# Optimization experiments

Hardware: AMD Instinct MI355X
Metric: run time of the kernel (lower is better)

Reference implementation:

```python
import jax, jax.numpy as jnp
import numpy as np

E = 64          # embedding_dim
H = 2 * E       # GRU hidden = input size = 128
ATT_HID = 36    # activation-unit MLP hidden


def _gru_scan(x, Wih, Whh, bih, bhh):
    """Standard (PyTorch-convention) GRU over x:[B,T,D] -> outputs [B,T,H]."""
    B = x.shape[0]
    gx = jnp.einsum('btd,gd->btg', x, Wih) + bih        # [B,T,3H], precompute input gates
    gx = jnp.swapaxes(gx, 0, 1)                          # [T,B,3H]
    h0 = jnp.zeros((B, H), x.dtype)

    def step(h, g):
        gh = h @ Whh.T + bhh                             # [B,3H]
        xr, xz, xn = jnp.split(g, 3, axis=-1)
        hr, hz, hn = jnp.split(gh, 3, axis=-1)
        r = jax.nn.sigmoid(xr + hr)
        z = jax.nn.sigmoid(xz + hz)
        n = jnp.tanh(xn + r * hn)
        h = (1.0 - z) * n + z * h
        return h, h

    _, hs = jax.lax.scan(step, h0, gx)                   # [T,B,H]
    return jnp.swapaxes(hs, 0, 1)                        # [B,T,H]


def _augru_scan(x, att, Wih, Whh, bih, bhh):
    """AUGRU: attention score scales the update gate. x:[B,T,H], att:[B,T]."""
    B = x.shape[0]
    gx = jnp.einsum('btd,gd->btg', x, Wih) + bih         # [B,T,3H]
    gx = jnp.swapaxes(gx, 0, 1)                          # [T,B,3H]
    a = jnp.swapaxes(att, 0, 1)[..., None]               # [T,B,1]
    h0 = jnp.zeros((B, H), x.dtype)

    def step(h, inp):
        g, at = inp
        gh = h @ Whh.T + bhh
        xr, xz, xn = jnp.split(g, 3, axis=-1)
        hr, hz, hn = jnp.split(gh, 3, axis=-1)
        r = jax.nn.sigmoid(xr + hr)
        u = jax.nn.sigmoid(xz + hz) * at                 # attention-modulated update gate
        n = jnp.tanh(xn + r * hn)
        h = (1.0 - u) * h + u * n
        return h, h

    _, hs = jax.lax.scan(step, h0, (gx, a))
    return jnp.swapaxes(hs, 0, 1)                        # [B,T,H]


def _attention_scores(query, hist, mask, W1, b1, W2, b2):
    """DIN activation unit: MLP over [q, h, q-h, q*h] -> masked softmax over T."""
    q = jnp.broadcast_to(query[:, None, :], hist.shape)  # [B,T,H]
    feat = jnp.concatenate([q, hist, q - hist, q * hist], axis=-1)  # [B,T,4H]
    hidden = jax.nn.sigmoid(jnp.einsum('btf,uf->btu', feat, W1) + b1)
    logits = (jnp.einsum('btu,ou->bto', hidden, W2) + b2)[..., 0]    # [B,T]
    logits = jnp.where(mask > 0, logits, -1e9)
    return jax.nn.softmax(logits, axis=-1)


def setup_inputs() -> dict:
    key = jax.random.key(0)
    ks = jax.random.split(key, 12)
    B, T = 1024, 200
    query_ad = jax.random.normal(ks[0], (B, H), jnp.float32)
    user_behavior = jax.random.normal(ks[1], (B, T, H), jnp.float32)
    lengths = jax.random.randint(ks[2], (B,), 1, T + 1)
    mask = (jnp.arange(T)[None, :] < lengths[:, None]).astype(jnp.int32)
    s = 1.0 / np.sqrt(H)
    p = {
        'gru_Wih': jax.random.uniform(ks[3], (3 * H, H), jnp.float32, -s, s),
        'gru_Whh': jax.random.uniform(ks[4], (3 * H, H), jnp.float32, -s, s),
        'gru_bih': jnp.zeros((3 * H,), jnp.float32),
        'gru_bhh': jnp.zeros((3 * H,), jnp.float32),
        'att_W1': jax.random.normal(ks[5], (ATT_HID, 4 * H), jnp.float32) * 0.05,
        'att_b1': jnp.zeros((ATT_HID,), jnp.float32),
        'att_W2': jax.random.normal(ks[6], (1, ATT_HID), jnp.float32) * 0.05,
        'att_b2': jnp.zeros((1,), jnp.float32),
        'augru_Wih': jax.random.uniform(ks[7], (3 * H, H), jnp.float32, -s, s),
        'augru_Whh': jax.random.uniform(ks[8], (3 * H, H), jnp.float32, -s, s),
        'augru_bih': jnp.zeros((3 * H,), jnp.float32),
        'augru_bhh': jnp.zeros((3 * H,), jnp.float32),
    }
    return dict(query_ad=query_ad, user_behavior=user_behavior, mask=mask, **p)


def reference(query_ad, user_behavior, mask,
              gru_Wih, gru_Whh, gru_bih, gru_bhh,
              att_W1, att_b1, att_W2, att_b2,
              augru_Wih, augru_Whh, augru_bih, augru_bhh):
    hist = _gru_scan(user_behavior, gru_Wih, gru_Whh, gru_bih, gru_bhh)       # [B,T,H]
    att = _attention_scores(query_ad, hist, mask, att_W1, att_b1, att_W2, att_b2)  # [B,T]
    out = _augru_scan(hist, att, augru_Wih, augru_Whh, augru_bih, augru_bhh)  # [B,T,H]
    lengths = jnp.sum(mask, axis=1)                                            # [B]
    B = out.shape[0]
    return out[jnp.arange(B), lengths - 1]                                     # [B,H]
```

## Files before the change

### kernel.cpp

```cpp
#include <hip/hip_runtime.h>

typedef _Float16 f16;
typedef _Float16 f16x8 __attribute__((ext_vector_type(8)));
typedef _Float16 f16x4 __attribute__((ext_vector_type(4)));
typedef float    f32x4 __attribute__((ext_vector_type(4)));

#define H  128
#define G3 384
#define AH 36
#define PADW 136

__device__ __forceinline__ float sigmoidf_(float x){
  return __builtin_amdgcn_rcpf(1.f + __expf(-x));
}
__device__ __forceinline__ float tanhf_(float x){
  return fmaf(2.f, __builtin_amdgcn_rcpf(1.f + __expf(-2.f*x)), -1.f);
}

__device__ __forceinline__ void lds_sync(){
  asm volatile("s_waitcnt lgkmcnt(0)" ::: "memory");
  __builtin_amdgcn_s_barrier();
  asm volatile("" ::: "memory");
}

__global__ void prep_weights(const float* __restrict__ a, const float* __restrict__ b,
                             const float* __restrict__ c, const float* __restrict__ d,
                             f16* __restrict__ dst)
{
  int i = blockIdx.x * 256 + threadIdx.x;
  if (i >= 4 * G3 * H) return;
  int m = i / (G3 * H), j = i % (G3 * H);
  const float* s = (m == 0) ? a : (m == 1) ? b : (m == 2) ? c : d;
  dst[i] = (f16)s[j];
}

__global__ void prep_len(const int* __restrict__ mask, int* __restrict__ len, int T, int B)
{
  int b = blockIdx.x * 256 + threadIdx.x;
  if (b >= B) return;
  int s = 0;
  for (int t = 0; t < T; ++t) s += (mask[(size_t)b * T + t] > 0);
  len[b] = s;
}

template<bool AUG>
__global__ __launch_bounds__(512)
__attribute__((amdgpu_waves_per_eu(2, 2)))
void scan_kernel(const float* __restrict__ xf32,
                 const f16*   __restrict__ xf16,
                 const f16*   __restrict__ Wih,
                 const f16*   __restrict__ Whh,
                 const float* __restrict__ bih,
                 const float* __restrict__ bhh,
                 const float* __restrict__ att,
                 const int*   __restrict__ len,
                 f16*         __restrict__ histo,
                 float*       __restrict__ outp,
                 int T)
{
  __shared__ f16  xs[2][16 * PADW];
  __shared__ f16  hs[2][16 * PADW];

  const int tid = threadIdx.x;
  const int w   = tid >> 6;
  const int l   = tid & 63;
  const int l16 = l & 15;
  const int lhi = l >> 4;
  const int b0  = blockIdx.x * 16;
  const int colb = w * 16;
  const int c4   = colb + lhi * 4;
  const int srow = tid >> 5, cc = tid & 31;

  f16x8 wih[3][4], whh[3][4];
  #pragma unroll
  for (int g = 0; g < 3; ++g)
    #pragma unroll
    for (int q = 0; q < 4; ++q) {
      int off = (g * H + colb + l16) * H + q * 32 + lhi * 8;
      wih[g][q] = *(const f16x8*)(Wih + off);
      whh[g][q] = *(const f16x8*)(Whh + off);
    }
  #pragma unroll
  for (int g = 0; g < 3; ++g)
    #pragma unroll
    for (int q = 0; q < 4; ++q)
      asm volatile("" : "+v"(wih[g][q]), "+v"(whh[g][q]));

  f32x4 bR  = *(const f32x4*)(bih + c4);
  { f32x4 t2 = *(const f32x4*)(bhh + c4);      bR  += t2; }
  f32x4 bZ  = *(const f32x4*)(bih + H + c4);
  { f32x4 t2 = *(const f32x4*)(bhh + H + c4);  bZ  += t2; }
  f32x4 bXn = *(const f32x4*)(bih + 2*H + c4);
  f32x4 bHn = *(const f32x4*)(bhh + 2*H + c4);

  float hold[4] = {0.f, 0.f, 0.f, 0.f};
  int len_l = 0;
  if (AUG) len_l = len[b0 + l16];

  const f16* xrd0 = &xs[0][l16 * PADW + lhi * 8];
  const f16* xrd1 = &xs[1][l16 * PADW + lhi * 8];
  const f16* hrd0 = &hs[0][l16 * PADW + lhi * 8];
  const f16* hrd1 = &hs[1][l16 * PADW + lhi * 8];
  f16* hwr0 = &hs[0][l16 * PADW + c4];
  f16* hwr1 = &hs[1][l16 * PADW + c4];
  f16* xst0 = &xs[0][srow * PADW + cc * 4];
  f16* xst1 = &xs[1][srow * PADW + cc * 4];

  const float* pxA32 = xf32 ? (xf32 + ((size_t)(b0 + srow) * T) * H + cc * 4) : nullptr;
  const f16*   pxA16 = xf16 ? (xf16 + ((size_t)(b0 + srow) * T) * H + cc * 4) : nullptr;
  const float* attB  = AUG ? (att + (size_t)(b0 + l16) * T) : nullptr;
  f16*         histp = (!AUG && histo) ? (histo + ((size_t)(b0 + l16) * T) * H + c4) : nullptr;
  float*       outpp = AUG ? (outp + (size_t)(b0 + l16) * H + c4) : nullptr;

  {
    f16x4 z4 = {(f16)0, (f16)0, (f16)0, (f16)0};
    *(f16x4*)(&hs[0][srow * PADW + cc * 4]) = z4;
    if (AUG) {
      f16x4 v = *(const f16x4*)(pxA16);
      *(f16x4*)xst0 = v;
    } else {
      f32x4 v = *(const f32x4*)(pxA32);
      f16x4 h4 = {(f16)v.x, (f16)v.y, (f16)v.z, (f16)v.w};
      *(f16x4*)xst0 = h4;
    }
  }
  f32x4 Pa32 = {0,0,0,0}, Pb32 = {0,0,0,0};
  f16x4 Pa16 = {(f16)0,(f16)0,(f16)0,(f16)0}, Pb16 = Pa16;
  float Aa = 0.f, Ab = 0.f;
  if (AUG) {
    Pa16 = *(const f16x4*)(pxA16 + H);
    Aa = attB[0];
    if (T > 1) Ab = attB[1];
  } else {
    Pa32 = *(const f32x4*)(pxA32 + H);
  }
  const float* pxE32 = pxA32 ? pxA32 + 2 * H : nullptr;
  const float* pxO32 = pxA32 ? pxA32 + 3 * H : nullptr;
  const f16*   pxE16 = pxA16 ? pxA16 + 2 * H : nullptr;
  const f16*   pxO16 = pxA16 ? pxA16 + 3 * H : nullptr;
  lds_sync();

#define STEP(targ_, XRD, HRD, HWRN, XSTN, PW32, PL32, PW16, PL16, AW, PXP32, PXP16) \
  {                                                                            \
    const int t5_  = (targ_);                                                  \
    float at_ = 0.f;                                                           \
    if (AUG) at_ = AW;                                                         \
    if (t5_ + 2 < T) {                                                         \
      if (AUG) {                                                               \
        PL16 = *(const f16x4*)(PXP16);  PXP16 += 2 * H;                        \
        AW = attB[t5_ + 2];                                                    \
      } else {                                                                 \
        PL32 = *(const f32x4*)(PXP32);  PXP32 += 2 * H;                        \
      }                                                                        \
    }                                                                          \
    f16x8 xb[4], hb[4];                                                        \
    _Pragma("unroll")                                                          \
    for (int q = 0; q < 4; ++q) {                                              \
      xb[q] = *(const f16x8*)(XRD + q * 32);                                   \
      hb[q] = *(const f16x8*)(HRD + q * 32);                                   \
    }                                                                          \
    f32x4 aR = bR, aZ = bZ, aXn = bXn, aHn = bHn;                              \
    _Pragma("unroll")                                                          \
    for (int q = 0; q < 4; ++q) {                                              \
      aR  = __builtin_amdgcn_mfma_f32_16x16x32_f16(wih[0][q], xb[q], aR, 0,0,0);  \
      aZ  = __builtin_amdgcn_mfma_f32_16x16x32_f16(wih[1][q], xb[q], aZ, 0,0,0);  \
      aXn = __builtin_amdgcn_mfma_f32_16x16x32_f16(wih[2][q], xb[q], aXn,0,0,0);  \
      aHn = __builtin_amdgcn_mfma_f32_16x16x32_f16(whh[2][q], hb[q], aHn,0,0,0);  \
    }                                                                          \
    _Pragma("unroll")                                                          \
    for (int q = 0; q < 4; ++q) {                                              \
      aR  = __builtin_amdgcn_mfma_f32_16x16x32_f16(whh[0][q], hb[q], aR, 0,0,0);  \
      aZ  = __builtin_amdgcn_mfma_f32_16x16x32_f16(whh[1][q], hb[q], aZ, 0,0,0);  \
    }                                                                          \
    float hn_[4];                                                              \
    _Pragma("unroll")                                                          \
    for (int i = 0; i < 4; ++i) {                                              \
      float r = sigmoidf_(aR[i]);                                              \
      float z = sigmoidf_(aZ[i]);                                              \
      float n = tanhf_(aXn[i] + r * aHn[i]);                                   \
      float h;                                                                 \
      if (AUG) { float u = z * at_; h = hold[i] + u * (n - hold[i]); }         \
      else     { h = n + z * (hold[i] - n); }                                  \
      hold[i] = h; hn_[i] = h;                                                 \
    }                                                                          \
    f16x4 hv = {(f16)hn_[0], (f16)hn_[1], (f16)hn_[2], (f16)hn_[3]};           \
    *(f16x4*)(HWRN) = hv;                                                      \
    if (!AUG) {                                                                \
      *(f16x4*)histp = hv;  histp += H;                                        \
    } else {                                                                   \
      if (t5_ == len_l - 1) {                                                  \
        f32x4 ov = {hn_[0], hn_[1], hn_[2], hn_[3]};                           \
        *(f32x4*)outpp = ov;                                                   \
      }                                                                        \
    }                                                                          \
    if (t5_ + 1 < T) {                                                         \
      if (AUG) {                                                               \
        *(f16x4*)(XSTN) = PW16;                                                \
      } else {                                                                 \
        f16x4 s4 = {(f16)PW32.x, (f16)PW32.y, (f16)PW32.z, (f16)PW32.w};       \
        *(f16x4*)(XSTN) = s4;                                                  \
      }                                                                        \
    }                                                                          \
    lds_sync();                                                                \
  }

  for (int t = 0; t < T; t += 2) {
    STEP(t,     xrd0, hrd0, hwr1, xst1, Pa32, Pb32, Pa16, Pb16, Aa, pxE32, pxE16)
    STEP(t + 1, xrd1, hrd1, hwr0, xst0, Pb32, Pa32, Pb16, Pa16, Ab, pxO32, pxO16)
  }
#undef STEP
}

__global__ __launch_bounds__(256)
void attn_kernel(const float* __restrict__ query,
                 const f16*   __restrict__ hist,
                 const int*   __restrict__ mask,
                 const float* __restrict__ W1, const float* __restrict__ b1,
                 const float* __restrict__ W2, const float* __restrict__ b2,
                 float* __restrict__ attv, int T)
{
  __shared__ float qs[H];
  __shared__ f16   WqH[48 * PADW];
  __shared__ float qcp[48], w2p[48];
  __shared__ float logitsS[224];
  __shared__ float red[256];

  const int tid = threadIdx.x, b = blockIdx.x;
  const int w = tid >> 6, l = tid & 63, l16 = l & 15, lhi = l >> 4;

  if (tid < H) qs[tid] = query[b * H + tid];
  if (tid < 48) w2p[tid] = (tid < AH) ? W2[tid] : 0.f;
  __syncthreads();

  for (int i = tid; i < 48 * H; i += 256) {
    int u = i >> 7, k = i & (H - 1);
    float v = 0.f;
    if (u < AH) {
      const float* r = W1 + u * 4 * H;
      v = r[H + k] - r[2*H + k] + qs[k] * r[3*H + k];
    }
    WqH[u * PADW + k] = (f16)v;
  }
  if (tid < 48) {
    float s = 0.f;
    if (tid < AH) {
      const float* r = W1 + tid * 4 * H;
      s = b1[tid];
      for (int k = 0; k < H; ++k) s += qs[k] * (r[k] + r[2*H + k]);
    }
    qcp[tid] = s;
  }
  __syncthreads();

  const f32x4 qcv0 = *(const f32x4*)&qcp[lhi*4];
  const f32x4 qcv1 = *(const f32x4*)&qcp[16 + lhi*4];
  const f32x4 qcv2 = *(const f32x4*)&qcp[32 + lhi*4];
  const f32x4 w2v0 = *(const f32x4*)&w2p[lhi*4];
  const f32x4 w2v1 = *(const f32x4*)&w2p[16 + lhi*4];
  const f32x4 w2v2 = *(const f32x4*)&w2p[32 + lhi*4];

  const int NMT = (T + 15) >> 4;
  for (int mt = w; mt < NMT; mt += 4) {
    const int t0 = mt * 16;
    f16x8 hbf[4];
    #pragma unroll
    for (int q = 0; q < 4; ++q)
      hbf[q] = *(const f16x8*)(hist + ((size_t)b*T + t0 + l16)*H + q*32 + lhi*8);
    f32x4 d0 = {0,0,0,0}, d1 = {0,0,0,0}, d2 = {0,0,0,0};
    #pragma unroll
    for (int q = 0; q < 4; ++q) {
      f16x8 wq0 = *(const f16x8*)(&WqH[ l16       * PADW + q*32 + lhi*8]);
      f16x8 wq1 = *(const f16x8*)(&WqH[(16 + l16) * PADW + q*32 + lhi*8]);
      f16x8 wq2 = *(const f16x8*)(&WqH[(32 + l16) * PADW + q*32 + lhi*8]);
      d0 = __builtin_amdgcn_mfma_f32_16x16x32_f16(wq0, hbf[q], d0, 0,0,0);
      d1 = __builtin_amdgcn_mfma_f32_16x16x32_f16(wq1, hbf[q], d1, 0,0,0);
      d2 = __builtin_amdgcn_mfma_f32_16x16x32_f16(wq2, hbf[q], d2, 0,0,0);
    }
    float p = 0.f;
    #pragma unroll
    for (int i = 0; i < 4; ++i) {
      p += w2v0[i] * sigmoidf_(d0[i] + qcv0[i]);
      p += w2v1[i] * sigmoidf_(d1[i] + qcv1[i]);
      p += w2v2[i] * sigmoidf_(d2[i] + qcv2[i]);
    }
    p += __shfl_xor(p, 16, 64);
    p += __shfl_xor(p, 32, 64);
    if (lhi == 0) logitsS[t0 + l16] = p;
  }
  __syncthreads();

  const int t = tid;
  float logit = -1e30f; int mk = 0;
  if (t < T) {
    mk = mask[(size_t)b*T + t];
    logit = (mk > 0) ? (logitsS[t] + b2[0]) : -1e30f;
  }
  red[tid] = logit; __syncthreads();
  for (int s = 128; s > 0; s >>= 1) { if (tid < s) red[tid] = fmaxf(red[tid], red[tid+s]); __syncthreads(); }
  float mx = red[0]; __syncthreads();
  float ev = (t < T && mk > 0) ? __expf(logit - mx) : 0.f;
  red[tid] = ev; __syncthreads();
  for (int s = 128; s > 0; s >>= 1) { if (tid < s) red[tid] += red[tid+s]; __syncthreads(); }
  float sm = red[0];
  if (t < T) attv[(size_t)b*T + t] = ev * __builtin_amdgcn_rcpf(sm);
}

extern "C" void kernel_launch(void* const* d_in, const int* in_sizes, int n_in,
                              void* d_out, int out_size, void* d_ws, size_t ws_size,
                              hipStream_t stream)
{
  const float* query = (const float*)d_in[0];
  const float* ub    = (const float*)d_in[1];
  const int*   mask  = (const int*)d_in[2];
  const float* gWih  = (const float*)d_in[3];
  const float* gWhh  = (const float*)d_in[4];
  const float* gbih  = (const float*)d_in[5];
  const float* gbhh  = (const float*)d_in[6];
  const float* aW1   = (const float*)d_in[7];
  const float* ab1   = (const float*)d_in[8];
  const float* aW2   = (const float*)d_in[9];
  const float* ab2   = (const float*)d_in[10];
  const float* uWih  = (const float*)d_in[11];
  const float* uWhh  = (const float*)d_in[12];
  const float* ubih  = (const float*)d_in[13];
  const float* ubhh  = (const float*)d_in[14];

  const int B = in_sizes[0] / H;
  const int T = in_sizes[1] / in_sizes[0];

  char*  ws   = (char*)d_ws;
  f16*   wf   = (f16*)ws;
  int*   lenp = (int*)(ws + 393216);
  float* attb = (float*)(ws + 397312);
  f16*   hist = (f16*)(ws + 397312 + (size_t)B * 200 * 4);

  prep_weights<<<(4 * G3 * H + 255) / 256, 256, 0, stream>>>(gWih, gWhh, uWih, uWhh, wf);
  prep_len<<<(B + 255) / 256, 256, 0, stream>>>(mask, lenp, T, B);

  scan_kernel<false><<<B / 16, 512, 0, stream>>>(
      ub, (const f16*)nullptr, wf, wf + G3 * H, gbih, gbhh,
      (const float*)nullptr, (const int*)nullptr, hist, (float*)nullptr, T);

  attn_kernel<<<B, 256, 0, stream>>>(query, hist, mask, aW1, ab1, aW2, ab2, attb, T);

  scan_kernel<true><<<B / 16, 512, 0, stream>>>(
      (const float*)nullptr, hist, wf + 2 * G3 * H, wf + 3 * G3 * H, ubih, ubhh,
      attb, lenp, (f16*)nullptr, (float*)d_out, T);
}
```

Before: 367.4 us.

## Move input-gate MFMAs off the recurrent critical path and load x directly into registers

The scan kernels now compute the input-projection MFMAs for step t+1 after the hidden-state update of step t, so each step's critical path only holds the three hidden-state MFMA chains. Input rows are loaded straight from global memory into MFMA operand registers, which removes the x LDS staging buffer and its stores. A new pre-pass converts user_behavior to fp16 into a workspace buffer. The cost is the extra conversion kernel, a larger workspace with hard-coded offsets, and higher register pressure from the double-buffered x fragments.

```diff
diff --git a/kernel.cpp b/kernel.cpp
--- a/kernel.cpp
+++ b/kernel.cpp
@@ -43,11 +43,23 @@
   len[b] = s;
 }
 
+__global__ __launch_bounds__(256)
+void prep_cvt(const float* __restrict__ src, f16* __restrict__ dst, int n8)
+{
+  int i = blockIdx.x * 256 + threadIdx.x;
+  const int stride = gridDim.x * 256;
+  for (; i < n8; i += stride) {
+    f32x4 a = *(const f32x4*)(src + (size_t)i * 8);
+    f32x4 b = *(const f32x4*)(src + (size_t)i * 8 + 4);
+    f16x8 o = {(f16)a.x,(f16)a.y,(f16)a.z,(f16)a.w,(f16)b.x,(f16)b.y,(f16)b.z,(f16)b.w};
+    *(f16x8*)(dst + (size_t)i * 8) = o;
+  }
+}
+
 template<bool AUG>
 __global__ __launch_bounds__(512)
 __attribute__((amdgpu_waves_per_eu(2, 2)))
-void scan_kernel(const float* __restrict__ xf32,
-                 const f16*   __restrict__ xf16,
+void scan_kernel(const f16*   __restrict__ xin,
                  const f16*   __restrict__ Wih,
                  const f16*   __restrict__ Whh,
                  const float* __restrict__ bih,
@@ -58,8 +70,7 @@
                  float*       __restrict__ outp,
                  int T)
 {
-  __shared__ f16  xs[2][16 * PADW];
-  __shared__ f16  hs[2][16 * PADW];
+  __shared__ f16 hs[2][16 * PADW];
 
   const int tid = threadIdx.x;
   const int w   = tid >> 6;
@@ -86,10 +97,10 @@
     for (int q = 0; q < 4; ++q)
       asm volatile("" : "+v"(wih[g][q]), "+v"(whh[g][q]));
 
-  f32x4 bR  = *(const f32x4*)(bih + c4);
-  { f32x4 t2 = *(const f32x4*)(bhh + c4);      bR  += t2; }
-  f32x4 bZ  = *(const f32x4*)(bih + H + c4);
-  { f32x4 t2 = *(const f32x4*)(bhh + H + c4);  bZ  += t2; }
+  f32x4 bRs = *(const f32x4*)(bih + c4);
+  { f32x4 t2 = *(const f32x4*)(bhh + c4);     bRs += t2; }
+  f32x4 bZs = *(const f32x4*)(bih + H + c4);
+  { f32x4 t2 = *(const f32x4*)(bhh + H + c4); bZs += t2; }
   f32x4 bXn = *(const f32x4*)(bih + 2*H + c4);
   f32x4 bHn = *(const f32x4*)(bhh + 2*H + c4);
 
@@ -97,87 +108,73 @@
   int len_l = 0;
   if (AUG) len_l = len[b0 + l16];
 
-  const f16* xrd0 = &xs[0][l16 * PADW + lhi * 8];
-  const f16* xrd1 = &xs[1][l16 * PADW + lhi * 8];
   const f16* hrd0 = &hs[0][l16 * PADW + lhi * 8];
   const f16* hrd1 = &hs[1][l16 * PADW + lhi * 8];
   f16* hwr0 = &hs[0][l16 * PADW + c4];
   f16* hwr1 = &hs[1][l16 * PADW + c4];
-  f16* xst0 = &xs[0][srow * PADW + cc * 4];
-  f16* xst1 = &xs[1][srow * PADW + cc * 4];
-
-  const float* pxA32 = xf32 ? (xf32 + ((size_t)(b0 + srow) * T) * H + cc * 4) : nullptr;
-  const f16*   pxA16 = xf16 ? (xf16 + ((size_t)(b0 + srow) * T) * H + cc * 4) : nullptr;
-  const float* attB  = AUG ? (att + (size_t)(b0 + l16) * T) : nullptr;
+
+  const f16*   pxF  = xin + ((size_t)(b0 + l16) * T) * H + lhi * 8;
+  const float* attB = AUG ? (att + (size_t)(b0 + l16) * T) : nullptr;
   f16*         histp = (!AUG && histo) ? (histo + ((size_t)(b0 + l16) * T) * H + c4) : nullptr;
   float*       outpp = AUG ? (outp + (size_t)(b0 + l16) * H + c4) : nullptr;
 
   {
     f16x4 z4 = {(f16)0, (f16)0, (f16)0, (f16)0};
     *(f16x4*)(&hs[0][srow * PADW + cc * 4]) = z4;
-    if (AUG) {
-      f16x4 v = *(const f16x4*)(pxA16);
-      *(f16x4*)xst0 = v;
-    } else {
-      f32x4 v = *(const f32x4*)(pxA32);
-      f16x4 h4 = {(f16)v.x, (f16)v.y, (f16)v.z, (f16)v.w};
-      *(f16x4*)xst0 = h4;
-    }
-  }
-  f32x4 Pa32 = {0,0,0,0}, Pb32 = {0,0,0,0};
-  f16x4 Pa16 = {(f16)0,(f16)0,(f16)0,(f16)0}, Pb16 = Pa16;
+  }
+  f32x4 aXr, aXz, aXn_;
+  {
+    f16x8 xb0[4];
+    #pragma unroll
+    for (int q = 0; q < 4; ++q) xb0[q] = *(const f16x8*)(pxF + q * 32);
+    aXr = bRs; aXz = bZs; aXn_ = bXn;
+    #pragma unroll
+    for (int q = 0; q < 4; ++q) {
+      aXr  = __builtin_amdgcn_mfma_f32_16x16x32_f16(wih[0][q], xb0[q], aXr, 0,0,0);
+      aXz  = __builtin_amdgcn_mfma_f32_16x16x32_f16(wih[1][q], xb0[q], aXz, 0,0,0);
+      aXn_ = __builtin_amdgcn_mfma_f32_16x16x32_f16(wih[2][q], xb0[q], aXn_,0,0,0);
+    }
+  }
+  f16x8 xbA[4], xbB[4];
+  if (T > 1) {
+    #pragma unroll
+    for (int q = 0; q < 4; ++q) xbA[q] = *(const f16x8*)(pxF + H + q * 32);
+  }
+  pxF += 2 * H;
   float Aa = 0.f, Ab = 0.f;
   if (AUG) {
-    Pa16 = *(const f16x4*)(pxA16 + H);
     Aa = attB[0];
     if (T > 1) Ab = attB[1];
-  } else {
-    Pa32 = *(const f32x4*)(pxA32 + H);
-  }
-  const float* pxE32 = pxA32 ? pxA32 + 2 * H : nullptr;
-  const float* pxO32 = pxA32 ? pxA32 + 3 * H : nullptr;
-  const f16*   pxE16 = pxA16 ? pxA16 + 2 * H : nullptr;
-  const f16*   pxO16 = pxA16 ? pxA16 + 3 * H : nullptr;
+  }
   lds_sync();
 
-#define STEP(targ_, XRD, HRD, HWRN, XSTN, PW32, PL32, PW16, PL16, AW, PXP32, PXP16) \
+#define STEP(targ_, XBW, XBL, HRD, HWRN, AW)                                   \
   {                                                                            \
-    const int t5_  = (targ_);                                                  \
+    const int t5_ = (targ_);                                                   \
     float at_ = 0.f;                                                           \
     if (AUG) at_ = AW;                                                         \
     if (t5_ + 2 < T) {                                                         \
-      if (AUG) {                                                               \
-        PL16 = *(const f16x4*)(PXP16);  PXP16 += 2 * H;                        \
-        AW = attB[t5_ + 2];                                                    \
-      } else {                                                                 \
-        PL32 = *(const f32x4*)(PXP32);  PXP32 += 2 * H;                        \
-      }                                                                        \
-    }                                                                          \
-    f16x8 xb[4], hb[4];                                                        \
+      _Pragma("unroll")                                                        \
+      for (int q = 0; q < 4; ++q) XBL[q] = *(const f16x8*)(pxF + q * 32);      \
+      if (AUG) AW = attB[t5_ + 2];                                             \
+    }                                                                          \
+    pxF += H;                                                                  \
+    f16x8 hb[4];                                                               \
+    _Pragma("unroll")                                                          \
+    for (int q = 0; q < 4; ++q) hb[q] = *(const f16x8*)(HRD + q * 32);         \
+    f32x4 aR = aXr, aZ = aXz, aN = bHn;                                        \
     _Pragma("unroll")                                                          \
     for (int q = 0; q < 4; ++q) {                                              \
-      xb[q] = *(const f16x8*)(XRD + q * 32);                                   \
-      hb[q] = *(const f16x8*)(HRD + q * 32);                                   \
-    }                                                                          \
-    f32x4 aR = bR, aZ = bZ, aXn = bXn, aHn = bHn;                              \
-    _Pragma("unroll")                                                          \
-    for (int q = 0; q < 4; ++q) {                                              \
-      aR  = __builtin_amdgcn_mfma_f32_16x16x32_f16(wih[0][q], xb[q], aR, 0,0,0);  \
-      aZ  = __builtin_amdgcn_mfma_f32_16x16x32_f16(wih[1][q], xb[q], aZ, 0,0,0);  \
-      aXn = __builtin_amdgcn_mfma_f32_16x16x32_f16(wih[2][q], xb[q], aXn,0,0,0);  \
-      aHn = __builtin_amdgcn_mfma_f32_16x16x32_f16(whh[2][q], hb[q], aHn,0,0,0);  \
-    }                                                                          \
-    _Pragma("unroll")                                                          \
-    for (int q = 0; q < 4; ++q) {                                              \
-      aR  = __builtin_amdgcn_mfma_f32_16x16x32_f16(whh[0][q], hb[q], aR, 0,0,0);  \
-      aZ  = __builtin_amdgcn_mfma_f32_16x16x32_f16(whh[1][q], hb[q], aZ, 0,0,0);  \
+      aR = __builtin_amdgcn_mfma_f32_16x16x32_f16(whh[0][q], hb[q], aR, 0,0,0);\
+      aZ = __builtin_amdgcn_mfma_f32_16x16x32_f16(whh[1][q], hb[q], aZ, 0,0,0);\
+      aN = __builtin_amdgcn_mfma_f32_16x16x32_f16(whh[2][q], hb[q], aN, 0,0,0);\
     }                                                                          \
     float hn_[4];                                                              \
     _Pragma("unroll")                                                          \
     for (int i = 0; i < 4; ++i) {                                              \
       float r = sigmoidf_(aR[i]);                                              \
       float z = sigmoidf_(aZ[i]);                                              \
-      float n = tanhf_(aXn[i] + r * aHn[i]);                                   \
+      float n = tanhf_(aXn_[i] + r * aN[i]);                                   \
       float h;                                                                 \
       if (AUG) { float u = z * at_; h = hold[i] + u * (n - hold[i]); }         \
       else     { h = n + z * (hold[i] - n); }                                  \
@@ -194,19 +191,20 @@
       }                                                                        \
     }                                                                          \
     if (t5_ + 1 < T) {                                                         \
-      if (AUG) {                                                               \
-        *(f16x4*)(XSTN) = PW16;                                                \
-      } else {                                                                 \
-        f16x4 s4 = {(f16)PW32.x, (f16)PW32.y, (f16)PW32.z, (f16)PW32.w};       \
-        *(f16x4*)(XSTN) = s4;                                                  \
+      aXr = bRs; aXz = bZs; aXn_ = bXn;                                        \
+      _Pragma("unroll")                                                        \
+      for (int q = 0; q < 4; ++q) {                                            \
+        aXr  = __builtin_amdgcn_mfma_f32_16x16x32_f16(wih[0][q], XBW[q], aXr, 0,0,0);  \
+        aXz  = __builtin_amdgcn_mfma_f32_16x16x32_f16(wih[1][q], XBW[q], aXz, 0,0,0);  \
+        aXn_ = __builtin_amdgcn_mfma_f32_16x16x32_f16(wih[2][q], XBW[q], aXn_,0,0,0);  \
       }                                                                        \
     }                                                                          \
     lds_sync();                                                                \
   }
 
   for (int t = 0; t < T; t += 2) {
-    STEP(t,     xrd0, hrd0, hwr1, xst1, Pa32, Pb32, Pa16, Pb16, Aa, pxE32, pxE16)
-    STEP(t + 1, xrd1, hrd1, hwr0, xst0, Pb32, Pa32, Pb16, Pa16, Ab, pxO32, pxO16)
+    STEP(t,     xbA, xbB, hrd0, hwr1, Aa)
+    STEP(t + 1, xbB, xbA, hrd1, hwr0, Ab)
   }
 #undef STEP
 }
@@ -328,22 +326,24 @@
   const int B = in_sizes[0] / H;
   const int T = in_sizes[1] / in_sizes[0];
 
-  char*  ws   = (char*)d_ws;
-  f16*   wf   = (f16*)ws;
-  int*   lenp = (int*)(ws + 393216);
-  float* attb = (float*)(ws + 397312);
-  f16*   hist = (f16*)(ws + 397312 + (size_t)B * 200 * 4);
+  char*  ws    = (char*)d_ws;
+  f16*   wf    = (f16*)ws;
+  int*   lenp  = (int*)(ws + 393216);
+  float* attb  = (float*)(ws + 397312);
+  f16*   hist  = (f16*)(ws + 1216512);
+  f16*   ubf16 = (f16*)(ws + 1216512 + 52428800);
 
   prep_weights<<<(4 * G3 * H + 255) / 256, 256, 0, stream>>>(gWih, gWhh, uWih, uWhh, wf);
   prep_len<<<(B + 255) / 256, 256, 0, stream>>>(mask, lenp, T, B);
+  prep_cvt<<<2048, 256, 0, stream>>>(ub, ubf16, B * T * H / 8);
 
   scan_kernel<false><<<B / 16, 512, 0, stream>>>(
-      ub, (const f16*)nullptr, wf, wf + G3 * H, gbih, gbhh,
+      ubf16, wf, wf + G3 * H, gbih, gbhh,
       (const float*)nullptr, (const int*)nullptr, hist, (float*)nullptr, T);
 
   attn_kernel<<<B, 256, 0, stream>>>(query, hist, mask, aW1, ab1, aW2, ab2, attb, T);
 
   scan_kernel<true><<<B / 16, 512, 0, stream>>>(
-      (const float*)nullptr, hist, wf + 2 * G3 * H, wf + 3 * G3 * H, ubih, ubhh,
+      hist, wf + 2 * G3 * H, wf + 3 * G3 * H, ubih, ubhh,
       attb, lenp, (f16*)nullptr, (float*)d_out, T);
 }
```

Measured after the change: 589.6 us. 1.6x slower.

## Halve scan block to 4 waves, each computing 32 hidden columns

Applied to the files above, without the earlier changes.

The recurrent scan kernel now runs 256 threads per block instead of 512, so each wave covers two 16-column tiles of the hidden state and keeps twice as many weight fragments in registers. The per-step LDS barrier then synchronises fewer waves, and staging loads are widened to 8 elements. In exchange, register pressure per wave doubles (96 f16x8 weight registers) and occupancy is forced to one wave per EU. The sequential MFMA chain per wave also grows, which may lengthen the per-step critical path.

```diff
diff --git a/kernel.cpp b/kernel.cpp
--- a/kernel.cpp
+++ b/kernel.cpp
@@ -4,6 +4,7 @@
 typedef _Float16 f16x8 __attribute__((ext_vector_type(8)));
 typedef _Float16 f16x4 __attribute__((ext_vector_type(4)));
 typedef float    f32x4 __attribute__((ext_vector_type(4)));
+typedef float    f32x8 __attribute__((ext_vector_type(8)));
 
 #define H  128
 #define G3 384
@@ -44,8 +45,8 @@
 }
 
 template<bool AUG>
-__global__ __launch_bounds__(512)
-__attribute__((amdgpu_waves_per_eu(2, 2)))
+__global__ __launch_bounds__(256)
+__attribute__((amdgpu_waves_per_eu(1, 1)))
 void scan_kernel(const float* __restrict__ xf32,
                  const f16*   __restrict__ xf16,
                  const f16*   __restrict__ Wih,
@@ -67,33 +68,44 @@
   const int l16 = l & 15;
   const int lhi = l >> 4;
   const int b0  = blockIdx.x * 16;
-  const int colb = w * 16;
-  const int c4   = colb + lhi * 4;
-  const int srow = tid >> 5, cc = tid & 31;
-
-  f16x8 wih[3][4], whh[3][4];
+  const int colb = w * 32;
+  const int c4a  = colb + lhi * 4;
+  const int srow = tid >> 4;
+  const int scol = (tid & 15) * 8;
+
+  f16x8 wih[3][2][4], whh[3][2][4];
   #pragma unroll
   for (int g = 0; g < 3; ++g)
     #pragma unroll
-    for (int q = 0; q < 4; ++q) {
-      int off = (g * H + colb + l16) * H + q * 32 + lhi * 8;
-      wih[g][q] = *(const f16x8*)(Wih + off);
-      whh[g][q] = *(const f16x8*)(Whh + off);
-    }
+    for (int c = 0; c < 2; ++c)
+      #pragma unroll
+      for (int q = 0; q < 4; ++q) {
+        int off = (g * H + colb + 16 * c + l16) * H + q * 32 + lhi * 8;
+        wih[g][c][q] = *(const f16x8*)(Wih + off);
+        whh[g][c][q] = *(const f16x8*)(Whh + off);
+      }
   #pragma unroll
   for (int g = 0; g < 3; ++g)
     #pragma unroll
-    for (int q = 0; q < 4; ++q)
-      asm volatile("" : "+v"(wih[g][q]), "+v"(whh[g][q]));
-
-  f32x4 bR  = *(const f32x4*)(bih + c4);
-  { f32x4 t2 = *(const f32x4*)(bhh + c4);      bR  += t2; }
-  f32x4 bZ  = *(const f32x4*)(bih + H + c4);
-  { f32x4 t2 = *(const f32x4*)(bhh + H + c4);  bZ  += t2; }
-  f32x4 bXn = *(const f32x4*)(bih + 2*H + c4);
-  f32x4 bHn = *(const f32x4*)(bhh + 2*H + c4);
-
-  float hold[4] = {0.f, 0.f, 0.f, 0.f};
+    for (int c = 0; c < 2; ++c)
+      #pragma unroll
+      for (int q = 0; q < 4; ++q)
+        asm volatile("" : "+v"(wih[g][c][q]), "+v"(whh[g][c][q]));
+
+  f32x4 bR0  = *(const f32x4*)(bih + c4a);
+  { f32x4 t2 = *(const f32x4*)(bhh + c4a);           bR0 += t2; }
+  f32x4 bR1  = *(const f32x4*)(bih + c4a + 16);
+  { f32x4 t2 = *(const f32x4*)(bhh + c4a + 16);      bR1 += t2; }
+  f32x4 bZ0  = *(const f32x4*)(bih + H + c4a);
+  { f32x4 t2 = *(const f32x4*)(bhh + H + c4a);       bZ0 += t2; }
+  f32x4 bZ1  = *(const f32x4*)(bih + H + c4a + 16);
+  { f32x4 t2 = *(const f32x4*)(bhh + H + c4a + 16);  bZ1 += t2; }
+  const f32x4 bXn0 = *(const f32x4*)(bih + 2*H + c4a);
+  const f32x4 bXn1 = *(const f32x4*)(bih + 2*H + c4a + 16);
+  const f32x4 bHn0 = *(const f32x4*)(bhh + 2*H + c4a);
+  const f32x4 bHn1 = *(const f32x4*)(bhh + 2*H + c4a + 16);
+
+  float hold0[4] = {0.f,0.f,0.f,0.f}, hold1[4] = {0.f,0.f,0.f,0.f};
   int len_l = 0;
   if (AUG) len_l = len[b0 + l16];
 
@@ -101,38 +113,37 @@
   const f16* xrd1 = &xs[1][l16 * PADW + lhi * 8];
   const f16* hrd0 = &hs[0][l16 * PADW + lhi * 8];
   const f16* hrd1 = &hs[1][l16 * PADW + lhi * 8];
-  f16* hwr0 = &hs[0][l16 * PADW + c4];
-  f16* hwr1 = &hs[1][l16 * PADW + c4];
-  f16* xst0 = &xs[0][srow * PADW + cc * 4];
-  f16* xst1 = &xs[1][srow * PADW + cc * 4];
-
-  const float* pxA32 = xf32 ? (xf32 + ((size_t)(b0 + srow) * T) * H + cc * 4) : nullptr;
-  const f16*   pxA16 = xf16 ? (xf16 + ((size_t)(b0 + srow) * T) * H + cc * 4) : nullptr;
+  f16* hwr0 = &hs[0][l16 * PADW + c4a];
+  f16* hwr1 = &hs[1][l16 * PADW + c4a];
+  f16* xst0 = &xs[0][srow * PADW + scol];
+  f16* xst1 = &xs[1][srow * PADW + scol];
+
+  const float* pxA32 = xf32 ? (xf32 + ((size_t)(b0 + srow) * T) * H + scol) : nullptr;
+  const f16*   pxA16 = xf16 ? (xf16 + ((size_t)(b0 + srow) * T) * H + scol) : nullptr;
   const float* attB  = AUG ? (att + (size_t)(b0 + l16) * T) : nullptr;
-  f16*         histp = (!AUG && histo) ? (histo + ((size_t)(b0 + l16) * T) * H + c4) : nullptr;
-  float*       outpp = AUG ? (outp + (size_t)(b0 + l16) * H + c4) : nullptr;
+  f16*         histp = (!AUG && histo) ? (histo + ((size_t)(b0 + l16) * T) * H + c4a) : nullptr;
+  float*       outpp = AUG ? (outp + (size_t)(b0 + l16) * H + c4a) : nullptr;
 
   {
-    f16x4 z4 = {(f16)0, (f16)0, (f16)0, (f16)0};
-    *(f16x4*)(&hs[0][srow * PADW + cc * 4]) = z4;
+    f16x8 z8 = {};
+    *(f16x8*)(&hs[0][srow * PADW + scol]) = z8;
     if (AUG) {
-      f16x4 v = *(const f16x4*)(pxA16);
-      *(f16x4*)xst0 = v;
+      *(f16x8*)xst0 = *(const f16x8*)(pxA16);
     } else {
-      f32x4 v = *(const f32x4*)(pxA32);
-      f16x4 h4 = {(f16)v.x, (f16)v.y, (f16)v.z, (f16)v.w};
-      *(f16x4*)xst0 = h4;
-    }
-  }
-  f32x4 Pa32 = {0,0,0,0}, Pb32 = {0,0,0,0};
-  f16x4 Pa16 = {(f16)0,(f16)0,(f16)0,(f16)0}, Pb16 = Pa16;
+      f32x8 v = *(const f32x8*)(pxA32);
+      f16x8 h8 = {(f16)v[0],(f16)v[1],(f16)v[2],(f16)v[3],(f16)v[4],(f16)v[5],(f16)v[6],(f16)v[7]};
+      *(f16x8*)xst0 = h8;
+    }
+  }
+  f32x8 Pa32 = {}, Pb32 = {};
+  f16x8 Pa16 = {}, Pb16 = {};
   float Aa = 0.f, Ab = 0.f;
   if (AUG) {
-    Pa16 = *(const f16x4*)(pxA16 + H);
+    if (T > 1) Pa16 = *(const f16x8*)(pxA16 + H);
     Aa = attB[0];
     if (T > 1) Ab = attB[1];
   } else {
-    Pa32 = *(const f32x4*)(pxA32 + H);
+    if (T > 1) Pa32 = *(const f32x8*)(pxA32 + H);
   }
   const float* pxE32 = pxA32 ? pxA32 + 2 * H : nullptr;
   const float* pxO32 = pxA32 ? pxA32 + 3 * H : nullptr;
@@ -147,10 +158,10 @@
     if (AUG) at_ = AW;                                                         \
     if (t5_ + 2 < T) {                                                         \
       if (AUG) {                                                               \
-        PL16 = *(const f16x4*)(PXP16);  PXP16 += 2 * H;                        \
+        PL16 = *(const f16x8*)(PXP16);  PXP16 += 2 * H;                        \
         AW = attB[t5_ + 2];                                                    \
       } else {                                                                 \
-        PL32 = *(const f32x4*)(PXP32);  PXP32 += 2 * H;                        \
+        PL32 = *(const f32x8*)(PXP32);  PXP32 += 2 * H;                        \
       }                                                                        \
     }                                                                          \
     f16x8 xb[4], hb[4];                                                        \
@@ -159,46 +170,70 @@
       xb[q] = *(const f16x8*)(XRD + q * 32);                                   \
       hb[q] = *(const f16x8*)(HRD + q * 32);                                   \
     }                                                                          \
-    f32x4 aR = bR, aZ = bZ, aXn = bXn, aHn = bHn;                              \
+    f32x4 aR0 = bR0, aR1 = bR1, aZ0 = bZ0, aZ1 = bZ1;                          \
+    f32x4 aXn0 = bXn0, aXn1 = bXn1, aHn0 = bHn0, aHn1 = bHn1;                  \
     _Pragma("unroll")                                                          \
     for (int q = 0; q < 4; ++q) {                                              \
-      aR  = __builtin_amdgcn_mfma_f32_16x16x32_f16(wih[0][q], xb[q], aR, 0,0,0);  \
-      aZ  = __builtin_amdgcn_mfma_f32_16x16x32_f16(wih[1][q], xb[q], aZ, 0,0,0);  \
-      aXn = __builtin_amdgcn_mfma_f32_16x16x32_f16(wih[2][q], xb[q], aXn,0,0,0);  \
-      aHn = __builtin_amdgcn_mfma_f32_16x16x32_f16(whh[2][q], hb[q], aHn,0,0,0);  \
+      aR0  = __builtin_amdgcn_mfma_f32_16x16x32_f16(wih[0][0][q], xb[q], aR0, 0,0,0); \
+      aR1  = __builtin_amdgcn_mfma_f32_16x16x32_f16(wih[0][1][q], xb[q], aR1, 0,0,0); \
+      aZ0  = __builtin_amdgcn_mfma_f32_16x16x32_f16(wih[1][0][q], xb[q], aZ0, 0,0,0); \
+      aZ1  = __builtin_amdgcn_mfma_f32_16x16x32_f16(wih[1][1][q], xb[q], aZ1, 0,0,0); \
+      aXn0 = __builtin_amdgcn_mfma_f32_16x16x32_f16(wih[2][0][q], xb[q], aXn0,0,0,0); \
+      aXn1 = __builtin_amdgcn_mfma_f32_16x16x32_f16(wih[2][1][q], xb[q], aXn1,0,0,0); \
+      aHn0 = __builtin_amdgcn_mfma_f32_16x16x32_f16(whh[2][0][q], hb[q], aHn0,0,0,0); \
+      aHn1 = __builtin_amdgcn_mfma_f32_16x16x32_f16(whh[2][1][q], hb[q], aHn1,0,0,0); \
     }                                                                          \
     _Pragma("unroll")                                                          \
     for (int q = 0; q < 4; ++q) {                                              \
-      aR  = __builtin_amdgcn_mfma_f32_16x16x32_f16(whh[0][q], hb[q], aR, 0,0,0);  \
-      aZ  = __builtin_amdgcn_mfma_f32_16x16x32_f16(whh[1][q], hb[q], aZ, 0,0,0);  \
-    }                                                                          \
-    float hn_[4];                                                              \
+      aR0 = __builtin_amdgcn_mfma_f32_16x16x32_f16(whh[0][0][q], hb[q], aR0, 0,0,0);  \
+      aR1 = __builtin_amdgcn_mfma_f32_16x16x32_f16(whh[0][1][q], hb[q], aR1, 0,0,0);  \
+      aZ0 = __builtin_amdgcn_mfma_f32_16x16x32_f16(whh[1][0][q], hb[q], aZ0, 0,0,0);  \
+      aZ1 = __builtin_amdgcn_mfma_f32_16x16x32_f16(whh[1][1][q], hb[q], aZ1, 0,0,0);  \
+    }                                                                          \
+    float hn0_[4], hn1_[4];                                                    \
     _Pragma("unroll")                                                          \
     for (int i = 0; i < 4; ++i) {                                              \
-      float r = sigmoidf_(aR[i]);                                              \
-      float z = sigmoidf_(aZ[i]);                                              \
-      float n = tanhf_(aXn[i] + r * aHn[i]);                                   \
+      float r = sigmoidf_(aR0[i]);                                             \
+      float z = sigmoidf_(aZ0[i]);                                             \
+      float n = tanhf_(aXn0[i] + r * aHn0[i]);                                 \
       float h;                                                                 \
-      if (AUG) { float u = z * at_; h = hold[i] + u * (n - hold[i]); }         \
-      else     { h = n + z * (hold[i] - n); }                                  \
-      hold[i] = h; hn_[i] = h;                                                 \
-    }                                                                          \
-    f16x4 hv = {(f16)hn_[0], (f16)hn_[1], (f16)hn_[2], (f16)hn_[3]};           \
-    *(f16x4*)(HWRN) = hv;                                                      \
+      if (AUG) { float u = z * at_; h = hold0[i] + u * (n - hold0[i]); }       \
+      else     { h = n + z * (hold0[i] - n); }                                 \
+      hold0[i] = h; hn0_[i] = h;                                               \
+    }                                                                          \
+    _Pragma("unroll")                                                          \
+    for (int i = 0; i < 4; ++i) {                                              \
+      float r = sigmoidf_(aR1[i]);                                             \
+      float z = sigmoidf_(aZ1[i]);                                             \
+      float n = tanhf_(aXn1[i] + r * aHn1[i]);                                 \
+      float h;                                                                 \
+      if (AUG) { float u = z * at_; h = hold1[i] + u * (n - hold1[i]); }       \
+      else     { h = n + z * (hold1[i] - n); }                                 \
+      hold1[i] = h; hn1_[i] = h;                                               \
+    }                                                                          \
+    f16x4 hv0 = {(f16)hn0_[0], (f16)hn0_[1], (f16)hn0_[2], (f16)hn0_[3]};      \
+    f16x4 hv1 = {(f16)hn1_[0], (f16)hn1_[1], (f16)hn1_[2], (f16)hn1_[3]};      \
+    *(f16x4*)(HWRN)      = hv0;                                                \
+    *(f16x4*)(HWRN + 16) = hv1;                                                \
     if (!AUG) {                                                                \
-      *(f16x4*)histp = hv;  histp += H;                                        \
+      *(f16x4*)(histp)      = hv0;                                             \
+      *(f16x4*)(histp + 16) = hv1;                                             \
+      histp += H;                                                              \
     } else {                                                                   \
       if (t5_ == len_l - 1) {                                                  \
-        f32x4 ov = {hn_[0], hn_[1], hn_[2], hn_[3]};                           \
-        *(f32x4*)outpp = ov;                                                   \
+        f32x4 o0 = {hn0_[0], hn0_[1], hn0_[2], hn0_[3]};                       \
+        f32x4 o1 = {hn1_[0], hn1_[1], hn1_[2], hn1_[3]};                       \
+        *(f32x4*)(outpp)      = o0;                                            \
+        *(f32x4*)(outpp + 16) = o1;                                            \
       }                                                                        \
     }                                                                          \
     if (t5_ + 1 < T) {                                                         \
       if (AUG) {                                                               \
-        *(f16x4*)(XSTN) = PW16;                                                \
+        *(f16x8*)(XSTN) = PW16;                                                \
       } else {                                                                 \
-        f16x4 s4 = {(f16)PW32.x, (f16)PW32.y, (f16)PW32.z, (f16)PW32.w};       \
-        *(f16x4*)(XSTN) = s4;                                                  \
+        f16x8 s8 = {(f16)PW32[0],(f16)PW32[1],(f16)PW32[2],(f16)PW32[3],       \
+                    (f16)PW32[4],(f16)PW32[5],(f16)PW32[6],(f16)PW32[7]};      \
+        *(f16x8*)(XSTN) = s8;                                                  \
       }                                                                        \
     }                                                                          \
     lds_sync();                                                                \
@@ -337,13 +372,13 @@
   prep_weights<<<(4 * G3 * H + 255) / 256, 256, 0, stream>>>(gWih, gWhh, uWih, uWhh, wf);
   prep_len<<<(B + 255) / 256, 256, 0, stream>>>(mask, lenp, T, B);
 
-  scan_kernel<false><<<B / 16, 512, 0, stream>>>(
+  scan_kernel<false><<<B / 16, 256, 0, stream>>>(
       ub, (const f16*)nullptr, wf, wf + G3 * H, gbih, gbhh,
       (const float*)nullptr, (const int*)nullptr, hist, (float*)nullptr, T);
 
   attn_kernel<<<B, 256, 0, stream>>>(query, hist, mask, aW1, ab1, aW2, ab2, attb, T);
 
-  scan_kernel<true><<<B / 16, 512, 0, stream>>>(
+  scan_kernel<true><<<B / 16, 256, 0, stream>>>(
       (const float*)nullptr, hist, wf + 2 * G3 * H, wf + 3 * G3 * H, ubih, ubhh,
       attb, lenp, (f16*)nullptr, (float*)d_out, T);
 }
```

After: 404.5 us. 1.1x slower.
